# Kernel optimization log

Hardware: AMD Instinct MI355X
Metric: run time of the kernel (lower is better)

The kernel has to match this reference:

```python
import jax, jax.numpy as jnp
import numpy as np

L, H, P = 16384, 1024, 512  # seq len, model width, state size (conj_sym: P = ssm_size//2)
DT_MIN, DT_MAX = 1e-3, 1e-1
STEP_RESCALE = 1.0


def setup_inputs() -> dict:
    key = jax.random.key(0)
    ks = jax.random.split(key, 7)
    input_sequence = jax.random.normal(ks[0], (L, H), dtype=jnp.float32)
    # Lambda: stable diagonal (Re < 0), like DPLR-HiPPO (Re = -0.5, spread imag parts)
    Lambda_re = -0.5 - jax.random.uniform(ks[1], (P,), dtype=jnp.float32)
    Lambda_im = 10.0 * jax.random.normal(ks[2], (P,), dtype=jnp.float32)
    # B (P,H,2) and C (H,P,2): real/imag stacked parameterization
    B = jax.random.normal(ks[3], (P, H, 2), dtype=jnp.float32) / np.float32(np.sqrt(H))
    C = jax.random.normal(ks[4], (H, P, 2), dtype=jnp.float32) / np.float32(np.sqrt(P))
    D = jax.random.normal(ks[5], (H,), dtype=jnp.float32)
    log_step = (jax.random.uniform(ks[6], (P, 1), dtype=jnp.float32)
                * (np.log(DT_MAX) - np.log(DT_MIN)) + np.log(DT_MIN)).astype(jnp.float32)
    return {"input_sequence": input_sequence, "Lambda_re": Lambda_re,
            "Lambda_im": Lambda_im, "B": B, "C": C, "D": D, "log_step": log_step}


def _binop(q_i, q_j):
    # diagonal linear recurrence composition; elementwise, so works on stacked arrays
    A_i, b_i = q_i
    A_j, b_j = q_j
    return (A_j * A_i, A_j * b_i + b_j)


def reference(input_sequence, Lambda_re, Lambda_im, B, C, D, log_step):
    Lambda = Lambda_re + 1j * Lambda_im                      # (P,) complex64
    B_tilde = B[..., 0] + 1j * B[..., 1]                     # (P,H)
    C_tilde = C[..., 0] + 1j * C[..., 1]                     # (H,P)
    Delta = STEP_RESCALE * jnp.exp(log_step[:, 0])           # (P,)
    # ZOH discretization
    Lambda_bar = jnp.exp(Lambda * Delta)                     # (P,)
    B_bar = ((Lambda_bar - 1.0) / Lambda)[:, None] * B_tilde # (P,H)
    # per-step scan elements
    Lambda_elements = jnp.broadcast_to(Lambda_bar, (input_sequence.shape[0], P))
    Bu_elements = jnp.einsum('lh,ph->lp', input_sequence, B_bar)  # (L,P) complex
    _, xs = jax.lax.associative_scan(_binop, (Lambda_elements, Bu_elements))
    # conj_sym readout: 2 * Re(C x)
    ys = 2.0 * jnp.einsum('lp,hp->lh', xs, C_tilde).real     # (L,H) float32
    return ys + input_sequence * D
```

## Files before the change

### kernel.cpp

```cpp
#include <hip/hip_runtime.h>
#include <math.h>

#define LL 16384
#define HH 1024
#define PP 512
#define NP2 1024
#define CHUNK 64
#define NCHUNK 256

#define BM2 256
#define BN2 256
#define SUBK 32
#define REG_U16 16384

typedef unsigned short u16;
typedef __attribute__((ext_vector_type(8))) short bf16x8;
typedef __attribute__((ext_vector_type(4))) float f32x4;

__device__ __forceinline__ u16 f2bf(float f) {
    unsigned u = __float_as_uint(f);
    unsigned r = 0x7fffu + ((u >> 16) & 1u);
    return (u16)((u + r) >> 16);
}
__device__ __forceinline__ float bf2f(u16 x) {
    return __uint_as_float(((unsigned)x) << 16);
}

__device__ __forceinline__ void gload_lds16(const void* g, void* l) {
    __builtin_amdgcn_global_load_lds(
        (const __attribute__((address_space(1))) unsigned int*)g,
        (__attribute__((address_space(3))) unsigned int*)l, 16, 0, 0);
}

__global__ void k_setup(const float* __restrict__ lre, const float* __restrict__ lim,
                        const float* __restrict__ logstep,
                        float* __restrict__ gre, float* __restrict__ gim,
                        float* __restrict__ lbre, float* __restrict__ lbim,
                        float* __restrict__ ltre, float* __restrict__ ltim) {
    int p = threadIdx.x;
    if (p >= PP) return;
    float dt = expf(logstep[p]);
    float ar = lre[p], ai = lim[p];
    float e = expf(ar * dt);
    float s, c;
    sincosf(ai * dt, &s, &c);
    float Lr = e * c, Li = e * s;
    lbre[p] = Lr; lbim[p] = Li;
    float nr = Lr - 1.0f, ni = Li;
    float den = ar * ar + ai * ai;
    gre[p] = (nr * ar + ni * ai) / den;
    gim[p] = (ni * ar - nr * ai) / den;
    float tr = Lr, ti = Li;
    for (int i = 0; i < 6; i++) {
        float rr = tr * tr - ti * ti;
        float mm = 2.0f * tr * ti;
        tr = rr; ti = mm;
    }
    ltre[p] = tr; ltim[p] = ti;
}

__global__ void k_prep2(const float* __restrict__ B,
                        const float* __restrict__ gre, const float* __restrict__ gim,
                        const float* __restrict__ C,
                        u16* __restrict__ bb, u16* __restrict__ cp) {
    if (blockIdx.x < 2048) {
        int t = blockIdx.x * 256 + threadIdx.x;
        int p = t >> 10, h = t & 1023;
        float2 b = ((const float2*)B)[t];
        float gr = gre[p], gi = gim[p];
        bb[(size_t)(2 * p) * HH + h]     = f2bf(gr * b.x - gi * b.y);
        bb[(size_t)(2 * p + 1) * HH + h] = f2bf(gr * b.y + gi * b.x);
    } else {
        int t = (blockIdx.x - 2048) * 256 + threadIdx.x;
        int h = t >> 9, p = t & 511;
        float2 c = ((const float2*)C)[t];
        cp[(size_t)h * NP2 + 2 * p]     = f2bf(c.x);
        cp[(size_t)h * NP2 + 2 * p + 1] = f2bf(-c.y);
    }
}

__global__ void k_cvt(const float* __restrict__ s, u16* __restrict__ d) {
    size_t i = ((size_t)blockIdx.x * 256 + threadIdx.x) * 4;
    float4 v = *(const float4*)&s[i];
    unsigned lo = (unsigned)f2bf(v.x) | ((unsigned)f2bf(v.y) << 16);
    unsigned hi = (unsigned)f2bf(v.z) | ((unsigned)f2bf(v.w) << 16);
    *(uint2*)&d[i] = make_uint2(lo, hi);
}

template<int FUSE>
__global__ __launch_bounds__(512, 2) void k_gemm2(
        const u16* __restrict__ A, const u16* __restrict__ Bt,
        void* __restrict__ outp, const int K,
        const u16* __restrict__ ubf, const float* __restrict__ Din,
        const float* __restrict__ lbre, const float* __restrict__ lbim,
        float* __restrict__ frO, float* __restrict__ fiO) {
    extern __shared__ u16 smem[];
    const int b = blockIdx.x;
    const int xcd = b & 7, sidx = b >> 3;
    const int m0 = (xcd * 8 + (sidx >> 2)) * BM2;
    const int n0 = (sidx & 3) * BN2;
    const int t = threadIdx.x;
    const int lane = t & 63, wid = t >> 6;
    const int wm = (wid >> 2) * 128, wn = (wid & 3) * 64;
    const int frow = lane & 15, quad = (lane >> 4) & 3;

    f32x4 acc[8][4];
    #pragma unroll
    for (int i = 0; i < 8; i++)
        #pragma unroll
        for (int j = 0; j < 4; j++) acc[i][j] = (f32x4){0.f, 0.f, 0.f, 0.f};

    const int sr = t >> 2, slot = t & 3;
    const int seg = slot ^ (sr & 3);
    const u16* gA = A + (size_t)(m0 + sr) * K + seg * 8;
    const u16* gB = Bt + (size_t)(n0 + sr) * K + seg * 8;
    const int ldst = sr * 32 + slot * 8;

    const int aoff = (wm + frow) * 32 + ((quad ^ (frow & 3)) * 8);
    const int boff = (wn + frow) * 32 + ((quad ^ (frow & 3)) * 8);

    const int NT = K / SUBK;

#define STAGE(k_) do {                                                  \
        u16* dst_ = smem + ((k_) & 3) * REG_U16 + ldst;                 \
        const u16* ga_ = gA + (k_) * SUBK;                              \
        const u16* gb_ = gB + (k_) * SUBK;                              \
        gload_lds16(ga_,                   dst_);                       \
        gload_lds16(ga_ + (size_t)128 * K, dst_ + 4096);                \
        gload_lds16(gb_,                   dst_ + 8192);                \
        gload_lds16(gb_ + (size_t)128 * K, dst_ + 12288);               \
    } while (0)

    STAGE(0); STAGE(1); STAGE(2);

    for (int s = 0; s < NT; ++s) {
        if (s + 3 < NT) STAGE(s + 3);
        if (s < NT - 2)       asm volatile("s_waitcnt vmcnt(8)" ::: "memory");
        else if (s == NT - 2) asm volatile("s_waitcnt vmcnt(4)" ::: "memory");
        else                  asm volatile("s_waitcnt vmcnt(0)" ::: "memory");
        asm volatile("s_barrier" ::: "memory");
        const u16* Ar = smem + (s & 3) * REG_U16;
        const u16* Br = Ar + 8192;
        bf16x8 av[8], bv[4];
        #pragma unroll
        for (int i = 0; i < 8; i++) av[i] = *(const bf16x8*)&Ar[aoff + i * 512];
        #pragma unroll
        for (int j = 0; j < 4; j++) bv[j] = *(const bf16x8*)&Br[boff + j * 512];
        __builtin_amdgcn_s_setprio(1);
        #pragma unroll
        for (int i = 0; i < 8; i++)
            #pragma unroll
            for (int j = 0; j < 4; j++)
                acc[i][j] = __builtin_amdgcn_mfma_f32_16x16x32_bf16(
                    av[i], bv[j], acc[i][j], 0, 0, 0);
        __builtin_amdgcn_s_setprio(0);
        asm volatile("s_barrier" ::: "memory");
    }
#undef STAGE

    if (FUSE) {
        float* Cout = (float*)outp;
        #pragma unroll
        for (int i = 0; i < 8; i++) {
            const int row = m0 + wm + i * 16 + quad * 4;
            #pragma unroll
            for (int j = 0; j < 4; j++) {
                const int col = n0 + wn + j * 16 + frow;
                const float dv = Din[col];
                f32x4 v = acc[i][j];
                #pragma unroll
                for (int r = 0; r < 4; r++) {
                    const size_t o = (size_t)(row + r) * 1024 + col;
                    Cout[o] = 2.0f * v[r] + bf2f(ubf[o]) * dv;
                }
            }
        }
    } else {
        u16* Cb = (u16*)outp;
        unsigned* sm32 = (unsigned*)smem;
        #pragma unroll
        for (int i = 0; i < 8; i++)
            #pragma unroll
            for (int j = 0; j < 4; j++) {
                f32x4 v = acc[i][j];
                #pragma unroll
                for (int r = 0; r < 4; r++)
                    smem[(wm + i * 16 + quad * 4 + r) * 256 + wn + j * 16 + frow]
                        = f2bf(v[r]);
            }
        __syncthreads();
        #pragma unroll
        for (int k = 0; k < 16; k++) {
            const int l = t + k * 512;
            const int row = l >> 5, c16 = (l & 31) * 8;
            *(uint4*)&Cb[(size_t)(m0 + row) * 1024 + n0 + c16] =
                ((const uint4*)smem)[l];
        }
        const int ch = t >> 7, q = t & 127;
        const int sp = (n0 >> 1) + q;
        const float sar = lbre[sp], sai = lbim[sp];
        float xr = 0.f, xi = 0.f;
        #pragma unroll 8
        for (int r = 0; r < 64; r++) {
            unsigned v = sm32[(ch * 64 + r) * 128 + q];
            float br = bf2f((u16)(v & 0xffff));
            float bi = bf2f((u16)(v >> 16));
            float nr = sar * xr - sai * xi + br;
            float ni = sar * xi + sai * xr + bi;
            xr = nr; xi = ni;
        }
        frO[((m0 >> 6) + ch) * PP + sp] = xr;
        fiO[((m0 >> 6) + ch) * PP + sp] = xi;
    }
}

__global__ __launch_bounds__(256) void k_scan2(
        const float* __restrict__ fr, const float* __restrict__ fi,
        const float* __restrict__ ltre, const float* __restrict__ ltim,
        float* __restrict__ cr, float* __restrict__ ci) {
    __shared__ float Ar[NCHUNK], Ai[NCHUNK], br[NCHUNK], bi[NCHUNK];
    const int p = blockIdx.x;
    const int c = threadIdx.x;
    const float lr = ltre[p], li = ltim[p];
    Ar[c] = lr; Ai[c] = li;
    br[c] = fr[c * PP + p];
    bi[c] = fi[c * PP + p];
    __syncthreads();
    #pragma unroll
    for (int d = 1; d < NCHUNK; d <<= 1) {
        float pAr = 0.f, pAi = 0.f, pbr = 0.f, pbi = 0.f;
        const bool has = (c >= d);
        if (has) { pAr = Ar[c-d]; pAi = Ai[c-d]; pbr = br[c-d]; pbi = bi[c-d]; }
        float cAr = Ar[c], cAi = Ai[c], cbr = br[c], cbi = bi[c];
        __syncthreads();
        if (has) {
            Ar[c] = cAr * pAr - cAi * pAi;
            Ai[c] = cAr * pAi + cAi * pAr;
            br[c] = cAr * pbr - cAi * pbi + cbr;
            bi[c] = cAr * pbi + cAi * pbr + cbi;
        }
        __syncthreads();
    }
    cr[c * PP + p] = (c == 0) ? 0.f : br[c-1];
    ci[c * PP + p] = (c == 0) ? 0.f : bi[c-1];
}

__global__ void k_scan3(unsigned* __restrict__ bu,
                        const float* __restrict__ lbre, const float* __restrict__ lbim,
                        const float* __restrict__ cr, const float* __restrict__ ci) {
    int p = blockIdx.x * 256 + threadIdx.x;
    int c = blockIdx.y;
    float ar = lbre[p], ai = lbim[p];
    float xr = cr[c * PP + p], xi = ci[c * PP + p];
    unsigned* b = bu + (size_t)c * CHUNK * PP + p;
    for (int j = 0; j < CHUNK; j += 4) {
        unsigned vv[4];
        vv[0] = b[0]; vv[1] = b[PP]; vv[2] = b[2 * PP]; vv[3] = b[3 * PP];
        unsigned w[4];
        #pragma unroll
        for (int q = 0; q < 4; q++) {
            float br = bf2f((u16)(vv[q] & 0xffff));
            float bi = bf2f((u16)(vv[q] >> 16));
            float nr = ar * xr - ai * xi + br;
            float ni = ar * xi + ai * xr + bi;
            xr = nr; xi = ni;
            w[q] = (unsigned)f2bf(xr) | ((unsigned)f2bf(xi) << 16);
        }
        b[0] = w[0]; b[PP] = w[1]; b[2 * PP] = w[2]; b[3 * PP] = w[3];
        b += 4 * PP;
    }
}

extern "C" void kernel_launch(void* const* d_in, const int* in_sizes, int n_in,
                              void* d_out, int out_size, void* d_ws, size_t ws_size,
                              hipStream_t stream) {
    const float* u       = (const float*)d_in[0];
    const float* lre     = (const float*)d_in[1];
    const float* lim     = (const float*)d_in[2];
    const float* B       = (const float*)d_in[3];
    const float* C       = (const float*)d_in[4];
    const float* D       = (const float*)d_in[5];
    const float* logstep = (const float*)d_in[6];
    float* out = (float*)d_out;

    float* w = (float*)d_ws;
    float* gre  = w;
    float* gim  = w + 512;
    float* lbre = w + 1024;
    float* lbim = w + 1536;
    float* ltre = w + 2048;
    float* ltim = w + 2560;
    float* fr   = w + 4096;
    float* fi   = fr + NCHUNK * PP;
    float* cr   = fi + NCHUNK * PP;
    float* ci   = cr + NCHUNK * PP;
    u16*   bub  = (u16*)(w + (1 << 20));
    u16*   ub   = bub + (size_t)LL * NP2;
    u16*   bb   = ub + (size_t)LL * HH;
    u16*   cp   = bb + (size_t)NP2 * HH;

    static int attr_done = 0;
    if (!attr_done) {
        hipFuncSetAttribute(reinterpret_cast<const void*>(k_gemm2<0>),
                            hipFuncAttributeMaxDynamicSharedMemorySize, 131072);
        hipFuncSetAttribute(reinterpret_cast<const void*>(k_gemm2<1>),
                            hipFuncAttributeMaxDynamicSharedMemorySize, 131072);
        attr_done = 1;
    }

    k_setup<<<1, 512, 0, stream>>>(lre, lim, logstep, gre, gim, lbre, lbim, ltre, ltim);
    k_prep2<<<4096, 256, 0, stream>>>(B, gre, gim, C, bb, cp);
    k_cvt<<<(LL * HH) / 1024, 256, 0, stream>>>(u, ub);
    k_gemm2<0><<<(NP2 / BN2) * (LL / BM2), 512, 131072, stream>>>(
        ub, bb, bub, HH, nullptr, nullptr, lbre, lbim, fr, fi);
    k_scan2<<<PP, NCHUNK, 0, stream>>>(fr, fi, ltre, ltim, cr, ci);
    k_scan3<<<dim3(PP / 256, NCHUNK), 256, 0, stream>>>(
        (unsigned*)bub, lbre, lbim, cr, ci);
    k_gemm2<1><<<(HH / BN2) * (LL / BM2), 512, 131072, stream>>>(
        bub, cp, out, NP2, ub, D, nullptr, nullptr, nullptr, nullptr);
}
```

Baseline: 244.7 us.

## Restructure GEMM main loop into interleaved half-phases with triple buffering

Rewrites the GEMM K-loop from a 4-buffer, 3-ahead prefetch into a 3-buffer, 2-ahead schedule. Each iteration is split into two phases that interleave LDS fragment reads, global-to-LDS prefetch issue and MFMA clusters, separated by sched_barriers and s_barriers. The LDS swizzle also changes to XOR on (row>>1)&3 to reduce bank conflicts. The goal is better overlap of memory and MFMA work, at the cost of more barriers per iteration and a shallower prefetch depth.

New measurement: 234.6 us. 1.04x faster.

```diff
diff --git a/kernel.cpp b/kernel.cpp
--- a/kernel.cpp
+++ b/kernel.cpp
@@ -31,6 +31,8 @@
         (const __attribute__((address_space(1))) unsigned int*)g,
         (__attribute__((address_space(3))) unsigned int*)l, 16, 0, 0);
 }
+
+#define SB0 __builtin_amdgcn_sched_barrier(0)
 
 __global__ void k_setup(const float* __restrict__ lre, const float* __restrict__ lim,
                         const float* __restrict__ logstep,
@@ -111,52 +113,120 @@
         for (int j = 0; j < 4; j++) acc[i][j] = (f32x4){0.f, 0.f, 0.f, 0.f};
 
     const int sr = t >> 2, slot = t & 3;
-    const int seg = slot ^ (sr & 3);
+    const int seg = slot ^ ((sr >> 1) & 3);
     const u16* gA = A + (size_t)(m0 + sr) * K + seg * 8;
     const u16* gB = Bt + (size_t)(n0 + sr) * K + seg * 8;
     const int ldst = sr * 32 + slot * 8;
 
-    const int aoff = (wm + frow) * 32 + ((quad ^ (frow & 3)) * 8);
-    const int boff = (wn + frow) * 32 + ((quad ^ (frow & 3)) * 8);
+    const int aoff = (wm + frow) * 32 + ((quad ^ ((frow >> 1) & 3)) * 8);
+    const int boff = (wn + frow) * 32 + ((quad ^ ((frow >> 1) & 3)) * 8);
 
     const int NT = K / SUBK;
 
-#define STAGE(k_) do {                                                  \
-        u16* dst_ = smem + ((k_) & 3) * REG_U16 + ldst;                 \
-        const u16* ga_ = gA + (k_) * SUBK;                              \
-        const u16* gb_ = gB + (k_) * SUBK;                              \
-        gload_lds16(ga_,                   dst_);                       \
-        gload_lds16(ga_ + (size_t)128 * K, dst_ + 4096);                \
-        gload_lds16(gb_,                   dst_ + 8192);                \
-        gload_lds16(gb_ + (size_t)128 * K, dst_ + 12288);               \
-    } while (0)
-
-    STAGE(0); STAGE(1); STAGE(2);
-
+    {
+        u16* d0 = smem + ldst;
+        gload_lds16(gA,                     d0);
+        gload_lds16(gA + (size_t)128 * K,   d0 + 4096);
+        gload_lds16(gB,                     d0 + 8192);
+        gload_lds16(gB + (size_t)128 * K,   d0 + 12288);
+        u16* d1 = smem + REG_U16 + ldst;
+        gload_lds16(gA + SUBK,                   d1);
+        gload_lds16(gA + (size_t)128 * K + SUBK, d1 + 4096);
+        gload_lds16(gB + SUBK,                   d1 + 8192);
+        gload_lds16(gB + (size_t)128 * K + SUBK, d1 + 12288);
+    }
+    asm volatile("s_waitcnt vmcnt(4)" ::: "memory");
+    SB0;
+    __builtin_amdgcn_s_barrier();
+    SB0;
+
+    int rc = 0;
+    int rs = 2;
     for (int s = 0; s < NT; ++s) {
-        if (s + 3 < NT) STAGE(s + 3);
-        if (s < NT - 2)       asm volatile("s_waitcnt vmcnt(8)" ::: "memory");
-        else if (s == NT - 2) asm volatile("s_waitcnt vmcnt(4)" ::: "memory");
-        else                  asm volatile("s_waitcnt vmcnt(0)" ::: "memory");
-        asm volatile("s_barrier" ::: "memory");
-        const u16* Ar = smem + (s & 3) * REG_U16;
+        const u16* Ar = smem + rc * REG_U16;
         const u16* Br = Ar + 8192;
-        bf16x8 av[8], bv[4];
-        #pragma unroll
-        for (int i = 0; i < 8; i++) av[i] = *(const bf16x8*)&Ar[aoff + i * 512];
-        #pragma unroll
-        for (int j = 0; j < 4; j++) bv[j] = *(const bf16x8*)&Br[boff + j * 512];
+        const bool do_stage = (s + 2 < NT);
+        const u16* gAs = gA + (size_t)(s + 2) * SUBK;
+        const u16* gBs = gB + (size_t)(s + 2) * SUBK;
+        u16* dS = smem + rs * REG_U16 + ldst;
+
+        bf16x8 av0 = *(const bf16x8*)&Ar[aoff + 0 * 512];
+        bf16x8 av1 = *(const bf16x8*)&Ar[aoff + 1 * 512];
+        bf16x8 av2 = *(const bf16x8*)&Ar[aoff + 2 * 512];
+        bf16x8 av3 = *(const bf16x8*)&Ar[aoff + 3 * 512];
+        bf16x8 bv0 = *(const bf16x8*)&Br[boff + 0 * 512];
+        bf16x8 bv1 = *(const bf16x8*)&Br[boff + 1 * 512];
+        bf16x8 bv2 = *(const bf16x8*)&Br[boff + 2 * 512];
+        bf16x8 bv3 = *(const bf16x8*)&Br[boff + 3 * 512];
+        if (do_stage) {
+            gload_lds16(gAs,                   dS);
+            gload_lds16(gAs + (size_t)128 * K, dS + 4096);
+        }
+        SB0;
+        __builtin_amdgcn_s_barrier();
+        asm volatile("s_waitcnt lgkmcnt(0)" ::: "memory");
+        SB0;
         __builtin_amdgcn_s_setprio(1);
-        #pragma unroll
-        for (int i = 0; i < 8; i++)
-            #pragma unroll
-            for (int j = 0; j < 4; j++)
-                acc[i][j] = __builtin_amdgcn_mfma_f32_16x16x32_bf16(
-                    av[i], bv[j], acc[i][j], 0, 0, 0);
+        acc[0][0] = __builtin_amdgcn_mfma_f32_16x16x32_bf16(av0, bv0, acc[0][0], 0, 0, 0);
+        acc[0][1] = __builtin_amdgcn_mfma_f32_16x16x32_bf16(av0, bv1, acc[0][1], 0, 0, 0);
+        acc[0][2] = __builtin_amdgcn_mfma_f32_16x16x32_bf16(av0, bv2, acc[0][2], 0, 0, 0);
+        acc[0][3] = __builtin_amdgcn_mfma_f32_16x16x32_bf16(av0, bv3, acc[0][3], 0, 0, 0);
+        acc[1][0] = __builtin_amdgcn_mfma_f32_16x16x32_bf16(av1, bv0, acc[1][0], 0, 0, 0);
+        acc[1][1] = __builtin_amdgcn_mfma_f32_16x16x32_bf16(av1, bv1, acc[1][1], 0, 0, 0);
+        acc[1][2] = __builtin_amdgcn_mfma_f32_16x16x32_bf16(av1, bv2, acc[1][2], 0, 0, 0);
+        acc[1][3] = __builtin_amdgcn_mfma_f32_16x16x32_bf16(av1, bv3, acc[1][3], 0, 0, 0);
+        acc[2][0] = __builtin_amdgcn_mfma_f32_16x16x32_bf16(av2, bv0, acc[2][0], 0, 0, 0);
+        acc[2][1] = __builtin_amdgcn_mfma_f32_16x16x32_bf16(av2, bv1, acc[2][1], 0, 0, 0);
+        acc[2][2] = __builtin_amdgcn_mfma_f32_16x16x32_bf16(av2, bv2, acc[2][2], 0, 0, 0);
+        acc[2][3] = __builtin_amdgcn_mfma_f32_16x16x32_bf16(av2, bv3, acc[2][3], 0, 0, 0);
+        acc[3][0] = __builtin_amdgcn_mfma_f32_16x16x32_bf16(av3, bv0, acc[3][0], 0, 0, 0);
+        acc[3][1] = __builtin_amdgcn_mfma_f32_16x16x32_bf16(av3, bv1, acc[3][1], 0, 0, 0);
+        acc[3][2] = __builtin_amdgcn_mfma_f32_16x16x32_bf16(av3, bv2, acc[3][2], 0, 0, 0);
+        acc[3][3] = __builtin_amdgcn_mfma_f32_16x16x32_bf16(av3, bv3, acc[3][3], 0, 0, 0);
         __builtin_amdgcn_s_setprio(0);
-        asm volatile("s_barrier" ::: "memory");
-    }
-#undef STAGE
+        SB0;
+        __builtin_amdgcn_s_barrier();
+        SB0;
+
+        bf16x8 av4 = *(const bf16x8*)&Ar[aoff + 4 * 512];
+        bf16x8 av5 = *(const bf16x8*)&Ar[aoff + 5 * 512];
+        bf16x8 av6 = *(const bf16x8*)&Ar[aoff + 6 * 512];
+        bf16x8 av7 = *(const bf16x8*)&Ar[aoff + 7 * 512];
+        if (do_stage) {
+            gload_lds16(gBs,                   dS + 8192);
+            gload_lds16(gBs + (size_t)128 * K, dS + 12288);
+        }
+        SB0;
+        __builtin_amdgcn_s_barrier();
+        asm volatile("s_waitcnt lgkmcnt(0)" ::: "memory");
+        SB0;
+        __builtin_amdgcn_s_setprio(1);
+        acc[4][0] = __builtin_amdgcn_mfma_f32_16x16x32_bf16(av4, bv0, acc[4][0], 0, 0, 0);
+        acc[4][1] = __builtin_amdgcn_mfma_f32_16x16x32_bf16(av4, bv1, acc[4][1], 0, 0, 0);
+        acc[4][2] = __builtin_amdgcn_mfma_f32_16x16x32_bf16(av4, bv2, acc[4][2], 0, 0, 0);
+        acc[4][3] = __builtin_amdgcn_mfma_f32_16x16x32_bf16(av4, bv3, acc[4][3], 0, 0, 0);
+        acc[5][0] = __builtin_amdgcn_mfma_f32_16x16x32_bf16(av5, bv0, acc[5][0], 0, 0, 0);
+        acc[5][1] = __builtin_amdgcn_mfma_f32_16x16x32_bf16(av5, bv1, acc[5][1], 0, 0, 0);
+        acc[5][2] = __builtin_amdgcn_mfma_f32_16x16x32_bf16(av5, bv2, acc[5][2], 0, 0, 0);
+        acc[5][3] = __builtin_amdgcn_mfma_f32_16x16x32_bf16(av5, bv3, acc[5][3], 0, 0, 0);
+        acc[6][0] = __builtin_amdgcn_mfma_f32_16x16x32_bf16(av6, bv0, acc[6][0], 0, 0, 0);
+        acc[6][1] = __builtin_amdgcn_mfma_f32_16x16x32_bf16(av6, bv1, acc[6][1], 0, 0, 0);
+        acc[6][2] = __builtin_amdgcn_mfma_f32_16x16x32_bf16(av6, bv2, acc[6][2], 0, 0, 0);
+        acc[6][3] = __builtin_amdgcn_mfma_f32_16x16x32_bf16(av6, bv3, acc[6][3], 0, 0, 0);
+        acc[7][0] = __builtin_amdgcn_mfma_f32_16x16x32_bf16(av7, bv0, acc[7][0], 0, 0, 0);
+        acc[7][1] = __builtin_amdgcn_mfma_f32_16x16x32_bf16(av7, bv1, acc[7][1], 0, 0, 0);
+        acc[7][2] = __builtin_amdgcn_mfma_f32_16x16x32_bf16(av7, bv2, acc[7][2], 0, 0, 0);
+        acc[7][3] = __builtin_amdgcn_mfma_f32_16x16x32_bf16(av7, bv3, acc[7][3], 0, 0, 0);
+        __builtin_amdgcn_s_setprio(0);
+        if (s < NT - 2)       asm volatile("s_waitcnt vmcnt(4)" ::: "memory");
+        else if (s == NT - 2) asm volatile("s_waitcnt vmcnt(0)" ::: "memory");
+        SB0;
+        __builtin_amdgcn_s_barrier();
+        SB0;
+
+        rc = (rc == 2) ? 0 : rc + 1;
+        rs = (rs == 2) ? 0 : rs + 1;
+    }
 
     if (FUSE) {
         float* Cout = (float*)outp;
```

## Use three-slot single-barrier LDS pipeline and change bank swizzle in GEMM

Applied to the files above, without the earlier changes.

The GEMM main loop moves from a 4-slot ring with two barriers per k-step and 3 tiles of prefetch to a 3-slot ring with one barrier per step and 2 tiles of prefetch. The next tile is issued after the barrier into the slot freed by the previous iteration. The LDS XOR swizzle now keys on (row>>1)&3 instead of row&3, aimed at reducing bank conflicts for the 16-byte fragment reads, and the s_setprio hints are removed. The shallower prefetch may expose more global-load latency, in exchange for one less barrier per step and lower LDS use.

Result: faster. 235.9 us (-3.6%).

```diff
diff --git a/kernel.cpp b/kernel.cpp
--- a/kernel.cpp
+++ b/kernel.cpp
@@ -111,52 +111,56 @@
         for (int j = 0; j < 4; j++) acc[i][j] = (f32x4){0.f, 0.f, 0.f, 0.f};
 
     const int sr = t >> 2, slot = t & 3;
-    const int seg = slot ^ (sr & 3);
+    const int seg = slot ^ ((sr >> 1) & 3);
     const u16* gA = A + (size_t)(m0 + sr) * K + seg * 8;
     const u16* gB = Bt + (size_t)(n0 + sr) * K + seg * 8;
     const int ldst = sr * 32 + slot * 8;
 
-    const int aoff = (wm + frow) * 32 + ((quad ^ (frow & 3)) * 8);
-    const int boff = (wn + frow) * 32 + ((quad ^ (frow & 3)) * 8);
+    const int aoff = (wm + frow) * 32 + ((quad ^ ((frow >> 1) & 3)) * 8);
+    const int boff = (wn + frow) * 32 + ((quad ^ ((frow >> 1) & 3)) * 8);
 
     const int NT = K / SUBK;
 
-#define STAGE(k_) do {                                                  \
-        u16* dst_ = smem + ((k_) & 3) * REG_U16 + ldst;                 \
-        const u16* ga_ = gA + (k_) * SUBK;                              \
-        const u16* gb_ = gB + (k_) * SUBK;                              \
+#define STAGE(slot_, k_) do {                                           \
+        u16* dst_ = smem + (slot_) * REG_U16 + ldst;                    \
+        const u16* ga_ = gA + (size_t)(k_) * SUBK;                      \
+        const u16* gb_ = gB + (size_t)(k_) * SUBK;                      \
         gload_lds16(ga_,                   dst_);                       \
         gload_lds16(ga_ + (size_t)128 * K, dst_ + 4096);                \
         gload_lds16(gb_,                   dst_ + 8192);                \
         gload_lds16(gb_ + (size_t)128 * K, dst_ + 12288);               \
     } while (0)
 
-    STAGE(0); STAGE(1); STAGE(2);
-
+    STAGE(0, 0);
+    STAGE(1, 1);
+
+    int rc = 0;
+    int rs = 2;
     for (int s = 0; s < NT; ++s) {
-        if (s + 3 < NT) STAGE(s + 3);
-        if (s < NT - 2)       asm volatile("s_waitcnt vmcnt(8)" ::: "memory");
-        else if (s == NT - 2) asm volatile("s_waitcnt vmcnt(4)" ::: "memory");
-        else                  asm volatile("s_waitcnt vmcnt(0)" ::: "memory");
-        asm volatile("s_barrier" ::: "memory");
-        const u16* Ar = smem + (s & 3) * REG_U16;
+        if (s == NT - 1) asm volatile("s_waitcnt vmcnt(0)" ::: "memory");
+        else             asm volatile("s_waitcnt vmcnt(4)" ::: "memory");
+        __builtin_amdgcn_s_barrier();
+        if (s + 2 < NT) STAGE(rs, s + 2);
+
+        const u16* Ar = smem + rc * REG_U16;
         const u16* Br = Ar + 8192;
         bf16x8 av[8], bv[4];
         #pragma unroll
         for (int i = 0; i < 8; i++) av[i] = *(const bf16x8*)&Ar[aoff + i * 512];
         #pragma unroll
         for (int j = 0; j < 4; j++) bv[j] = *(const bf16x8*)&Br[boff + j * 512];
-        __builtin_amdgcn_s_setprio(1);
         #pragma unroll
         for (int i = 0; i < 8; i++)
             #pragma unroll
             for (int j = 0; j < 4; j++)
                 acc[i][j] = __builtin_amdgcn_mfma_f32_16x16x32_bf16(
                     av[i], bv[j], acc[i][j], 0, 0, 0);
-        __builtin_amdgcn_s_setprio(0);
-        asm volatile("s_barrier" ::: "memory");
+
+        rc = (rc == 2) ? 0 : rc + 1;
+        rs = (rs == 2) ? 0 : rs + 1;
     }
 #undef STAGE
+    __builtin_amdgcn_s_barrier();
 
     if (FUSE) {
         float* Cout = (float*)outp;
```
